# Kernel tuning notes

Measured on AMD Instinct MI355X. Metric: run time of the kernel, lower is better.

The kernel has to match this reference:

```python
import jax, jax.numpy as jnp
import numpy as np

B, E, D_IN, D = 4096, 8, 768, 768  # batch, num_domains, bert hidden, d_model


def setup_inputs() -> dict:
    key = jax.random.key(0)
    ks = jax.random.split(key, 10)
    rn = lambda k, sh: jax.random.normal(k, sh, dtype=jnp.float32) * 0.02
    zeros = lambda sh: jnp.zeros(sh, dtype=jnp.float32)
    return {
        "pooled": jax.random.normal(ks[0], (B, D_IN), dtype=jnp.float32),
        "domain_ids": jax.random.randint(ks[1], (B,), 0, E),
        # text_feature_extractor: Linear(768, d_model) + ReLU
        "W_tfe": rn(ks[2], (D_IN, D)), "b_tfe": zeros((D,)),
        # DomainFeatureExtractor per domain: FFN_1, FFN_2 (d->d each)
        "W1": rn(ks[3], (E, D, D)), "b1": zeros((E, D)),
        "W2": rn(ks[4], (E, D, D)), "b2": zeros((E, D)),
        # AdaptiveGate per domain: linear_1, linear_2 (d->d), gate_linear (2d->1)
        "G1": rn(ks[5], (E, D, D)), "g1b": zeros((E, D)),
        "G2": rn(ks[6], (E, D, D)), "g2b": zeros((E, D)),
        "Gg": rn(ks[7], (E, 2 * D)), "ggb": zeros((E,)),
    }


def reference(pooled, domain_ids, W_tfe, b_tfe, W1, b1, W2, b2,
              G1, g1b, G2, g2b, Gg, ggb):
    # text feature extractor (dropout = identity in eval)
    x = jax.nn.relu(pooled @ W_tfe + b_tfe)                        # [B, D]

    # Dense dispatch: compute every expert for every sample, then select.
    # Same math as the per-sample python loop in the torch module.
    h = jax.nn.relu(jnp.einsum('bd,edh->beh', x, W1) + b1)         # [B, E, D]
    df = jnp.einsum('beh,ehk->bek', h, W2) + b2                    # [B, E, D]

    # AdaptiveGate
    t = jax.nn.relu(jnp.einsum('bd,edh->beh', x, G1) + g1b)        # [B, E, D]
    dr = jax.nn.relu(jnp.einsum('bed,edh->beh', df, G2) + g2b)     # [B, E, D]
    # gate_linear on concat([t, dr]) == t @ Gg[:, :D] + dr @ Gg[:, D:]
    gl = (jnp.einsum('bed,ed->be', t, Gg[:, :D])
          + jnp.einsum('bed,ed->be', dr, Gg[:, D:]) + ggb)         # [B, E]
    gate = jax.nn.sigmoid(gl)                                      # [B, E]

    # route: pick this sample's domain expert
    b_idx = jnp.arange(x.shape[0])
    df_s = df[b_idx, domain_ids]                                   # [B, D]
    g_s = gate[b_idx, domain_ids][:, None]                         # [B, 1]

    final_feature = g_s * df_s + (1.0 - g_s) * x                   # [B, D]
    return final_feature
```

## Files before the change

kernel.cpp:

```cpp
#include <hip/hip_runtime.h>
#include <stdint.h>

#define BATCH 4096
#define NEXP 8
#define DIM 768
#define BM 128
#define BN 128
#define BK 32
#define MAXROWS (BATCH + NEXP * BM)
#define ROWBLKS (MAXROWS / BM)
#define COLBLKS (DIM / BN)
#define MATELEMS (DIM * DIM)

typedef __attribute__((ext_vector_type(4))) float f32x4;
typedef __attribute__((ext_vector_type(8))) __bf16 bf16x8;
typedef __attribute__((ext_vector_type(8))) unsigned short ushort8v;
typedef __attribute__((ext_vector_type(4))) unsigned short ushort4v;

__device__ __forceinline__ unsigned short f2bf(float f) {
  union { float f; unsigned u; } v; v.f = f;
  unsigned r = v.u + 0x7FFFu + ((v.u >> 16) & 1u);
  return (unsigned short)(r >> 16);
}
__device__ __forceinline__ float bf2f(unsigned short h) {
  union { unsigned u; float f; } v; v.u = ((unsigned)h) << 16;
  return v.f;
}

__global__ __launch_bounds__(256) void k_cvt(const float* __restrict__ src,
                                             unsigned short* __restrict__ dst, int n4) {
  int i = blockIdx.x * 256 + threadIdx.x;
  if (i >= n4) return;
  float4 v = *(const float4*)(src + (size_t)i * 4);
  ushort4v o = { f2bf(v.x), f2bf(v.y), f2bf(v.z), f2bf(v.w) };
  *(ushort4v*)(dst + (size_t)i * 4) = o;
}

__global__ __launch_bounds__(256) void k_transpose(
    const float* __restrict__ Wtfe, const float* __restrict__ W1,
    const float* __restrict__ W2, const float* __restrict__ G1,
    const float* __restrict__ G2, unsigned short* __restrict__ dst)
{
  __shared__ unsigned short lds[64][72];
  const int m = blockIdx.y;
  const float* src;
  if (m == 0)      src = Wtfe;
  else if (m < 9)  src = W1 + (size_t)(m - 1) * MATELEMS;
  else if (m < 17) src = W2 + (size_t)(m - 9) * MATELEMS;
  else if (m < 25) src = G1 + (size_t)(m - 17) * MATELEMS;
  else             src = G2 + (size_t)(m - 25) * MATELEMS;
  unsigned short* d = dst + (size_t)m * MATELEMS;
  const int r0 = (blockIdx.x / 12) * 64;
  const int c0 = (blockIdx.x % 12) * 64;
  const int t = threadIdx.x;
#pragma unroll
  for (int p = 0; p < 4; ++p) {
    int ri = p * 16 + (t >> 4);
    int ci = (t & 15) * 4;
    float4 v = *(const float4*)(src + (size_t)(r0 + ri) * DIM + c0 + ci);
    lds[ri][ci + 0] = f2bf(v.x);
    lds[ri][ci + 1] = f2bf(v.y);
    lds[ri][ci + 2] = f2bf(v.z);
    lds[ri][ci + 3] = f2bf(v.w);
  }
  __syncthreads();
#pragma unroll
  for (int p = 0; p < 2; ++p) {
    int jj = p * 32 + (t >> 3);
    int ii0 = (t & 7) * 8;
    ushort8v o;
#pragma unroll
    for (int u = 0; u < 8; ++u) o[u] = lds[ii0 + u][jj];
    *(ushort8v*)(d + (size_t)(c0 + jj) * DIM + r0 + ii0) = o;
  }
}

__global__ __launch_bounds__(256) void k_sort(const int* __restrict__ dom,
                                              int* __restrict__ seg,
                                              int* __restrict__ perm,
                                              float* __restrict__ gl) {
  __shared__ int cnt[8], cur[8], pstart[9];
  const int t = threadIdx.x;
  if (t < 8) { cnt[t] = 0; cur[t] = 0; }
  __syncthreads();
  for (int b = t; b < BATCH; b += 256) atomicAdd(&cnt[dom[b]], 1);
  __syncthreads();
  if (t == 0) {
    int acc = 0;
    for (int e = 0; e < 8; ++e) {
      pstart[e] = acc;
      acc += (cnt[e] + BM - 1) / BM * BM;
    }
    pstart[8] = acc;
    for (int e = 0; e < 9; ++e) seg[e] = pstart[e];
    for (int e = 0; e < 8; ++e) seg[9 + e] = cnt[e];
  }
  __syncthreads();
  for (int i = t; i < MAXROWS; i += 256) { perm[i] = 0; gl[i] = 0.0f; }
  __syncthreads();
  for (int b = t; b < BATCH; b += 256) {
    int e = dom[b];
    int pos = pstart[e] + atomicAdd(&cur[e], 1);
    perm[pos] = b;
  }
}

template <int MODE>
__global__ __launch_bounds__(256) void k_gemm(
    const unsigned short* __restrict__ A,
    const unsigned short* __restrict__ Wt,
    const float* __restrict__ bias,
    const float* __restrict__ Gg,
    const int* __restrict__ seg,
    const int* __restrict__ perm,
    unsigned short* __restrict__ Out,
    float* __restrict__ gl)
{
  __shared__ __align__(16) unsigned short lA[BM * BK];
  __shared__ __align__(16) unsigned short lB[BN * BK];

  const int i0 = blockIdx.x * BM;
  const int total = seg[8];
  if (i0 >= total) return;
  int e = 0;
#pragma unroll
  for (int q = 1; q < 8; ++q) if (i0 >= seg[q]) e = q;

  const int n0 = blockIdx.y * BN;
  const int t = threadIdx.x;
  const int lane = t & 63;
  const int w = t >> 6;
  const int wr = w >> 1, wc = w & 1;

  const unsigned short* We = Wt + (size_t)(MODE == 0 ? 0 : e) * MATELEMS;

  int grow[2];
#pragma unroll
  for (int c = 0; c < 2; ++c) {
    int sub = w * 2 + c;
    int row = sub * 16 + (lane >> 2);
    grow[c] = (MODE == 0) ? perm[i0 + row] : (i0 + row);
  }
  const int colb = (lane & 3) * 8;

  f32x4 acc[4][4];
#pragma unroll
  for (int mi = 0; mi < 4; ++mi)
#pragma unroll
    for (int ni = 0; ni < 4; ++ni) acc[mi][ni] = f32x4{0.f, 0.f, 0.f, 0.f};

  for (int kk = 0; kk < DIM; kk += BK) {
    ushort8v ta[2], tb[2];
#pragma unroll
    for (int c = 0; c < 2; ++c) {
      int sub = w * 2 + c;
      int brow = n0 + sub * 16 + (lane >> 2);
      ta[c] = *(const ushort8v*)(A + (size_t)grow[c] * DIM + kk + colb);
      tb[c] = *(const ushort8v*)(We + (size_t)brow * DIM + kk + colb);
    }
    __syncthreads();
#pragma unroll
    for (int c = 0; c < 2; ++c) {
      int sub = w * 2 + c;
      *(ushort8v*)(lA + sub * 512 + lane * 8) = ta[c];
      *(ushort8v*)(lB + sub * 512 + lane * 8) = tb[c];
    }
    __syncthreads();

    const int fr = lane & 15;
    const int kg = (lane >> 4) * 8;
    bf16x8 af[4], bfr[4];
#pragma unroll
    for (int mi = 0; mi < 4; ++mi) {
      ushort8v raw = *(const ushort8v*)(lA + (wr * 64 + mi * 16 + fr) * BK + kg);
      af[mi] = __builtin_bit_cast(bf16x8, raw);
    }
#pragma unroll
    for (int ni = 0; ni < 4; ++ni) {
      ushort8v raw = *(const ushort8v*)(lB + (wc * 64 + ni * 16 + fr) * BK + kg);
      bfr[ni] = __builtin_bit_cast(bf16x8, raw);
    }
#pragma unroll
    for (int mi = 0; mi < 4; ++mi)
#pragma unroll
      for (int ni = 0; ni < 4; ++ni)
        acc[mi][ni] = __builtin_amdgcn_mfma_f32_16x16x32_bf16(af[mi], bfr[ni], acc[mi][ni], 0, 0, 0);
  }

  const int fr = lane & 15;
  const int rg = (lane >> 4) * 4;

  if constexpr (MODE <= 2) {
#pragma unroll
    for (int mi = 0; mi < 4; ++mi) {
#pragma unroll
      for (int ni = 0; ni < 4; ++ni) {
        int gcol = n0 + wc * 64 + ni * 16 + fr;
        float bv = (MODE == 0) ? bias[gcol] : bias[e * DIM + gcol];
#pragma unroll
        for (int r = 0; r < 4; ++r) {
          int go = i0 + wr * 64 + mi * 16 + rg + r;
          float v = acc[mi][ni][r] + bv;
          if (MODE != 2) v = fmaxf(v, 0.0f);
          Out[(size_t)go * DIM + gcol] = f2bf(v);
        }
      }
    }
  } else {
    float psum[4][4];
#pragma unroll
    for (int mi = 0; mi < 4; ++mi)
#pragma unroll
      for (int r = 0; r < 4; ++r) psum[mi][r] = 0.0f;
#pragma unroll
    for (int mi = 0; mi < 4; ++mi) {
#pragma unroll
      for (int ni = 0; ni < 4; ++ni) {
        int gcol = n0 + wc * 64 + ni * 16 + fr;
        float bv = bias[e * DIM + gcol];
        float gg = Gg[e * 2 * DIM + (MODE == 4 ? DIM : 0) + gcol];
#pragma unroll
        for (int r = 0; r < 4; ++r) {
          float v = fmaxf(acc[mi][ni][r] + bv, 0.0f);
          psum[mi][r] += v * gg;
        }
      }
    }
#pragma unroll
    for (int s = 1; s < 16; s <<= 1)
#pragma unroll
      for (int mi = 0; mi < 4; ++mi)
#pragma unroll
        for (int r = 0; r < 4; ++r)
          psum[mi][r] += __shfl_xor(psum[mi][r], s, 64);
    if ((lane & 15) == 0) {
#pragma unroll
      for (int mi = 0; mi < 4; ++mi)
#pragma unroll
        for (int r = 0; r < 4; ++r)
          atomicAdd(&gl[i0 + wr * 64 + mi * 16 + rg + r], psum[mi][r]);
    }
  }
}

__global__ __launch_bounds__(256) void k_blend(
    const int* __restrict__ seg, const int* __restrict__ perm,
    const float* __restrict__ gl, const float* __restrict__ ggb,
    const unsigned short* __restrict__ xbf, const unsigned short* __restrict__ dfbf,
    float* __restrict__ out)
{
  int idx = blockIdx.x * 256 + threadIdx.x;
  int i = idx / 192;
  int q = idx % 192;
  if (i >= seg[8]) return;
  int e = 0;
#pragma unroll
  for (int p = 1; p < 8; ++p) if (i >= seg[p]) e = p;
  if (i - seg[e] >= seg[9 + e]) return;
  int b = perm[i];
  float z = gl[i] + ggb[e];
  float g = 1.0f / (1.0f + __expf(-z));
  ushort4v dv = *(const ushort4v*)(dfbf + (size_t)i * DIM + q * 4);
  ushort4v xv = *(const ushort4v*)(xbf + (size_t)i * DIM + q * 4);
  float4 o;
  o.x = g * bf2f(dv[0]) + (1.0f - g) * bf2f(xv[0]);
  o.y = g * bf2f(dv[1]) + (1.0f - g) * bf2f(xv[1]);
  o.z = g * bf2f(dv[2]) + (1.0f - g) * bf2f(xv[2]);
  o.w = g * bf2f(dv[3]) + (1.0f - g) * bf2f(xv[3]);
  *(float4*)(out + (size_t)b * DIM + q * 4) = o;
}

extern "C" void kernel_launch(void* const* d_in, const int* in_sizes, int n_in,
                              void* d_out, int out_size, void* d_ws, size_t ws_size,
                              hipStream_t stream)
{
  const float* pooled = (const float*)d_in[0];
  const int*   dom    = (const int*)d_in[1];
  const float* Wtfe   = (const float*)d_in[2];
  const float* btfe   = (const float*)d_in[3];
  const float* W1     = (const float*)d_in[4];
  const float* b1     = (const float*)d_in[5];
  const float* W2     = (const float*)d_in[6];
  const float* b2     = (const float*)d_in[7];
  const float* G1     = (const float*)d_in[8];
  const float* g1b    = (const float*)d_in[9];
  const float* G2     = (const float*)d_in[10];
  const float* g2b    = (const float*)d_in[11];
  const float* Gg     = (const float*)d_in[12];
  const float* ggb    = (const float*)d_in[13];
  float* out = (float*)d_out;

  char* w = (char*)d_ws;
  size_t o = 0;
  auto alloc = [&](size_t bytes) { char* p = w + o; o += (bytes + 255) & ~(size_t)255; return p; };
  int*            seg  = (int*)alloc(64 * 4);
  int*            perm = (int*)alloc(MAXROWS * 4);
  float*          gl   = (float*)alloc(MAXROWS * 4);
  unsigned short* pbf  = (unsigned short*)alloc((size_t)BATCH * DIM * 2);
  unsigned short* wt   = (unsigned short*)alloc((size_t)33 * MATELEMS * 2);
  unsigned short* xbf  = (unsigned short*)alloc((size_t)MAXROWS * DIM * 2);
  unsigned short* hbf  = (unsigned short*)alloc((size_t)MAXROWS * DIM * 2);
  unsigned short* dfbf = (unsigned short*)alloc((size_t)MAXROWS * DIM * 2);
  if (o > ws_size) return;

  k_cvt<<<(BATCH * DIM / 4 + 255) / 256, 256, 0, stream>>>(pooled, pbf, BATCH * DIM / 4);
  k_transpose<<<dim3(144, 33), 256, 0, stream>>>(Wtfe, W1, W2, G1, G2, wt);
  k_sort<<<1, 256, 0, stream>>>(dom, seg, perm, gl);

  dim3 gg(ROWBLKS, COLBLKS);
  k_gemm<0><<<gg, 256, 0, stream>>>(pbf,  wt,                          btfe, nullptr, seg, perm, xbf,  nullptr);
  k_gemm<1><<<gg, 256, 0, stream>>>(xbf,  wt + (size_t)1  * MATELEMS,  b1,   nullptr, seg, perm, hbf,  nullptr);
  k_gemm<2><<<gg, 256, 0, stream>>>(hbf,  wt + (size_t)9  * MATELEMS,  b2,   nullptr, seg, perm, dfbf, nullptr);
  k_gemm<3><<<gg, 256, 0, stream>>>(xbf,  wt + (size_t)17 * MATELEMS,  g1b,  Gg,      seg, perm, nullptr, gl);
  k_gemm<4><<<gg, 256, 0, stream>>>(dfbf, wt + (size_t)25 * MATELEMS,  g2b,  Gg,      seg, perm, nullptr, gl);

  k_blend<<<(MAXROWS * 192 + 255) / 256, 256, 0, stream>>>(seg, perm, gl, ggb, xbf, dfbf, out);
}
```

Before: 268.4 us.

## Fuse pooled conversion into first GEMM, merge FFN1 with gate GEMM, halve BM

The separate fp32-to-bf16 conversion kernel is removed, and the first GEMM now loads fp32 pooled rows directly and converts them in registers. The FFN_1 and gate linear_1 GEMMs, which both read x, are merged into one launch with a doubled column grid that picks the weight set per block. The row tile shrinks from 128 to 64, which cuts per-expert padding and doubles the block count. The cost is smaller per-block MFMA tiles with less A/B reuse, plus a strided fp32 gather in the first GEMM.

```diff
diff --git a/kernel.cpp b/kernel.cpp
--- a/kernel.cpp
+++ b/kernel.cpp
@@ -4,12 +4,11 @@
 #define BATCH 4096
 #define NEXP 8
 #define DIM 768
-#define BM 128
+#define BM 64
 #define BN 128
 #define BK 32
 #define MAXROWS (BATCH + NEXP * BM)
 #define ROWBLKS (MAXROWS / BM)
-#define COLBLKS (DIM / BN)
 #define MATELEMS (DIM * DIM)
 
 typedef __attribute__((ext_vector_type(4))) float f32x4;
@@ -25,15 +24,6 @@
 __device__ __forceinline__ float bf2f(unsigned short h) {
   union { unsigned u; float f; } v; v.u = ((unsigned)h) << 16;
   return v.f;
-}
-
-__global__ __launch_bounds__(256) void k_cvt(const float* __restrict__ src,
-                                             unsigned short* __restrict__ dst, int n4) {
-  int i = blockIdx.x * 256 + threadIdx.x;
-  if (i >= n4) return;
-  float4 v = *(const float4*)(src + (size_t)i * 4);
-  ushort4v o = { f2bf(v.x), f2bf(v.y), f2bf(v.z), f2bf(v.w) };
-  *(ushort4v*)(dst + (size_t)i * 4) = o;
 }
 
 __global__ __launch_bounds__(256) void k_transpose(
@@ -107,9 +97,11 @@
 
 template <int MODE>
 __global__ __launch_bounds__(256) void k_gemm(
-    const unsigned short* __restrict__ A,
-    const unsigned short* __restrict__ Wt,
-    const float* __restrict__ bias,
+    const void* __restrict__ Ain,
+    const unsigned short* __restrict__ Wa,
+    const float* __restrict__ ba,
+    const unsigned short* __restrict__ Wb,
+    const float* __restrict__ bb,
     const float* __restrict__ Gg,
     const int* __restrict__ seg,
     const int* __restrict__ perm,
@@ -120,86 +112,99 @@
   __shared__ __align__(16) unsigned short lB[BN * BK];
 
   const int i0 = blockIdx.x * BM;
-  const int total = seg[8];
-  if (i0 >= total) return;
+  if (i0 >= seg[8]) return;
   int e = 0;
 #pragma unroll
   for (int q = 1; q < 8; ++q) if (i0 >= seg[q]) e = q;
 
-  const int n0 = blockIdx.y * BN;
+  const bool isgate = (MODE == 3) || (MODE == 1 && blockIdx.y >= 6);
+  const int n0 = (MODE == 1 ? (int)(blockIdx.y % 6) : (int)blockIdx.y) * BN;
+
+  const unsigned short* We;
+  const float* bias;
+  if (MODE == 0) { We = Wa; bias = ba; }
+  else if (MODE == 1) {
+    We = (isgate ? Wb : Wa) + (size_t)e * MATELEMS;
+    bias = (isgate ? bb : ba) + e * DIM;
+  } else {
+    We = Wa + (size_t)e * MATELEMS;
+    bias = ba + e * DIM;
+  }
+
   const int t = threadIdx.x;
   const int lane = t & 63;
   const int w = t >> 6;
   const int wr = w >> 1, wc = w & 1;
-
-  const unsigned short* We = Wt + (size_t)(MODE == 0 ? 0 : e) * MATELEMS;
-
-  int grow[2];
-#pragma unroll
-  for (int c = 0; c < 2; ++c) {
-    int sub = w * 2 + c;
-    int row = sub * 16 + (lane >> 2);
-    grow[c] = (MODE == 0) ? perm[i0 + row] : (i0 + row);
-  }
+  const int srow = lane >> 2;
   const int colb = (lane & 3) * 8;
 
-  f32x4 acc[4][4];
-#pragma unroll
-  for (int mi = 0; mi < 4; ++mi)
+  const int arow_l = w * 16 + srow;
+  const int garow = (MODE == 0) ? perm[i0 + arow_l] : (i0 + arow_l);
+
+  const unsigned short* Abf = (const unsigned short*)Ain;
+  const float* Af32 = (const float*)Ain;
+
+  const int fr = lane & 15;
+  const int sl = lane >> 4;
+  const int kg = sl * 8;
+
+  f32x4 acc[2][4];
+#pragma unroll
+  for (int mi = 0; mi < 2; ++mi)
 #pragma unroll
     for (int ni = 0; ni < 4; ++ni) acc[mi][ni] = f32x4{0.f, 0.f, 0.f, 0.f};
 
   for (int kk = 0; kk < DIM; kk += BK) {
-    ushort8v ta[2], tb[2];
+    ushort8v ta, tb[2];
+    if (MODE == 0) {
+      float4 va0 = *(const float4*)(Af32 + (size_t)garow * DIM + kk + colb);
+      float4 va1 = *(const float4*)(Af32 + (size_t)garow * DIM + kk + colb + 4);
+      ta = ushort8v{ f2bf(va0.x), f2bf(va0.y), f2bf(va0.z), f2bf(va0.w),
+                     f2bf(va1.x), f2bf(va1.y), f2bf(va1.z), f2bf(va1.w) };
+    } else {
+      ta = *(const ushort8v*)(Abf + (size_t)garow * DIM + kk + colb);
+    }
 #pragma unroll
     for (int c = 0; c < 2; ++c) {
-      int sub = w * 2 + c;
-      int brow = n0 + sub * 16 + (lane >> 2);
-      ta[c] = *(const ushort8v*)(A + (size_t)grow[c] * DIM + kk + colb);
+      int brow = n0 + (w * 2 + c) * 16 + srow;
       tb[c] = *(const ushort8v*)(We + (size_t)brow * DIM + kk + colb);
     }
     __syncthreads();
-#pragma unroll
-    for (int c = 0; c < 2; ++c) {
-      int sub = w * 2 + c;
-      *(ushort8v*)(lA + sub * 512 + lane * 8) = ta[c];
-      *(ushort8v*)(lB + sub * 512 + lane * 8) = tb[c];
-    }
+    *(ushort8v*)(lA + arow_l * 32 + colb) = ta;
+#pragma unroll
+    for (int c = 0; c < 2; ++c)
+      *(ushort8v*)(lB + ((w * 2 + c) * 16 + srow) * 32 + colb) = tb[c];
     __syncthreads();
 
-    const int fr = lane & 15;
-    const int kg = (lane >> 4) * 8;
-    bf16x8 af[4], bfr[4];
-#pragma unroll
-    for (int mi = 0; mi < 4; ++mi) {
-      ushort8v raw = *(const ushort8v*)(lA + (wr * 64 + mi * 16 + fr) * BK + kg);
+    bf16x8 af[2], bfv[4];
+#pragma unroll
+    for (int mi = 0; mi < 2; ++mi) {
+      ushort8v raw = *(const ushort8v*)(lA + (wr * 32 + mi * 16 + fr) * 32 + kg);
       af[mi] = __builtin_bit_cast(bf16x8, raw);
     }
 #pragma unroll
     for (int ni = 0; ni < 4; ++ni) {
-      ushort8v raw = *(const ushort8v*)(lB + (wc * 64 + ni * 16 + fr) * BK + kg);
-      bfr[ni] = __builtin_bit_cast(bf16x8, raw);
-    }
-#pragma unroll
-    for (int mi = 0; mi < 4; ++mi)
+      ushort8v raw = *(const ushort8v*)(lB + (wc * 64 + ni * 16 + fr) * 32 + kg);
+      bfv[ni] = __builtin_bit_cast(bf16x8, raw);
+    }
+#pragma unroll
+    for (int mi = 0; mi < 2; ++mi)
 #pragma unroll
       for (int ni = 0; ni < 4; ++ni)
-        acc[mi][ni] = __builtin_amdgcn_mfma_f32_16x16x32_bf16(af[mi], bfr[ni], acc[mi][ni], 0, 0, 0);
-  }
-
-  const int fr = lane & 15;
-  const int rg = (lane >> 4) * 4;
-
-  if constexpr (MODE <= 2) {
-#pragma unroll
-    for (int mi = 0; mi < 4; ++mi) {
+        acc[mi][ni] = __builtin_amdgcn_mfma_f32_16x16x32_bf16(af[mi], bfv[ni], acc[mi][ni], 0, 0, 0);
+  }
+
+  const int rg = sl * 4;
+  if (!isgate) {
+#pragma unroll
+    for (int mi = 0; mi < 2; ++mi) {
 #pragma unroll
       for (int ni = 0; ni < 4; ++ni) {
         int gcol = n0 + wc * 64 + ni * 16 + fr;
-        float bv = (MODE == 0) ? bias[gcol] : bias[e * DIM + gcol];
+        float bv = bias[gcol];
 #pragma unroll
         for (int r = 0; r < 4; ++r) {
-          int go = i0 + wr * 64 + mi * 16 + rg + r;
+          int go = i0 + wr * 32 + mi * 16 + rg + r;
           float v = acc[mi][ni][r] + bv;
           if (MODE != 2) v = fmaxf(v, 0.0f);
           Out[(size_t)go * DIM + gcol] = f2bf(v);
@@ -207,38 +212,37 @@
       }
     }
   } else {
-    float psum[4][4];
-#pragma unroll
-    for (int mi = 0; mi < 4; ++mi)
+    const int goff = (MODE == 3) ? DIM : 0;
+    float psum[2][4];
+#pragma unroll
+    for (int mi = 0; mi < 2; ++mi)
 #pragma unroll
       for (int r = 0; r < 4; ++r) psum[mi][r] = 0.0f;
 #pragma unroll
-    for (int mi = 0; mi < 4; ++mi) {
+    for (int mi = 0; mi < 2; ++mi) {
 #pragma unroll
       for (int ni = 0; ni < 4; ++ni) {
         int gcol = n0 + wc * 64 + ni * 16 + fr;
-        float bv = bias[e * DIM + gcol];
-        float gg = Gg[e * 2 * DIM + (MODE == 4 ? DIM : 0) + gcol];
-#pragma unroll
-        for (int r = 0; r < 4; ++r) {
-          float v = fmaxf(acc[mi][ni][r] + bv, 0.0f);
-          psum[mi][r] += v * gg;
-        }
+        float bv = bias[gcol];
+        float gg = Gg[e * 2 * DIM + goff + gcol];
+#pragma unroll
+        for (int r = 0; r < 4; ++r)
+          psum[mi][r] += fmaxf(acc[mi][ni][r] + bv, 0.0f) * gg;
       }
     }
 #pragma unroll
     for (int s = 1; s < 16; s <<= 1)
 #pragma unroll
-      for (int mi = 0; mi < 4; ++mi)
+      for (int mi = 0; mi < 2; ++mi)
 #pragma unroll
         for (int r = 0; r < 4; ++r)
           psum[mi][r] += __shfl_xor(psum[mi][r], s, 64);
-    if ((lane & 15) == 0) {
-#pragma unroll
-      for (int mi = 0; mi < 4; ++mi)
+    if (fr == 0) {
+#pragma unroll
+      for (int mi = 0; mi < 2; ++mi)
 #pragma unroll
         for (int r = 0; r < 4; ++r)
-          atomicAdd(&gl[i0 + wr * 64 + mi * 16 + rg + r], psum[mi][r]);
+          atomicAdd(&gl[i0 + wr * 32 + mi * 16 + rg + r], psum[mi][r]);
     }
   }
 }
@@ -296,23 +300,25 @@
   int*            seg  = (int*)alloc(64 * 4);
   int*            perm = (int*)alloc(MAXROWS * 4);
   float*          gl   = (float*)alloc(MAXROWS * 4);
-  unsigned short* pbf  = (unsigned short*)alloc((size_t)BATCH * DIM * 2);
   unsigned short* wt   = (unsigned short*)alloc((size_t)33 * MATELEMS * 2);
   unsigned short* xbf  = (unsigned short*)alloc((size_t)MAXROWS * DIM * 2);
   unsigned short* hbf  = (unsigned short*)alloc((size_t)MAXROWS * DIM * 2);
   unsigned short* dfbf = (unsigned short*)alloc((size_t)MAXROWS * DIM * 2);
   if (o > ws_size) return;
 
-  k_cvt<<<(BATCH * DIM / 4 + 255) / 256, 256, 0, stream>>>(pooled, pbf, BATCH * DIM / 4);
   k_transpose<<<dim3(144, 33), 256, 0, stream>>>(Wtfe, W1, W2, G1, G2, wt);
   k_sort<<<1, 256, 0, stream>>>(dom, seg, perm, gl);
 
-  dim3 gg(ROWBLKS, COLBLKS);
-  k_gemm<0><<<gg, 256, 0, stream>>>(pbf,  wt,                          btfe, nullptr, seg, perm, xbf,  nullptr);
-  k_gemm<1><<<gg, 256, 0, stream>>>(xbf,  wt + (size_t)1  * MATELEMS,  b1,   nullptr, seg, perm, hbf,  nullptr);
-  k_gemm<2><<<gg, 256, 0, stream>>>(hbf,  wt + (size_t)9  * MATELEMS,  b2,   nullptr, seg, perm, dfbf, nullptr);
-  k_gemm<3><<<gg, 256, 0, stream>>>(xbf,  wt + (size_t)17 * MATELEMS,  g1b,  Gg,      seg, perm, nullptr, gl);
-  k_gemm<4><<<gg, 256, 0, stream>>>(dfbf, wt + (size_t)25 * MATELEMS,  g2b,  Gg,      seg, perm, nullptr, gl);
+  const unsigned short* wt0  = wt;
+  const unsigned short* wt1  = wt + (size_t)1  * MATELEMS;
+  const unsigned short* wt2  = wt + (size_t)9  * MATELEMS;
+  const unsigned short* wtg1 = wt + (size_t)17 * MATELEMS;
+  const unsigned short* wtg2 = wt + (size_t)25 * MATELEMS;
+
+  k_gemm<0><<<dim3(ROWBLKS, 6),  256, 0, stream>>>(pooled, wt0,  btfe, nullptr, nullptr, Gg, seg, perm, xbf,  gl);
+  k_gemm<1><<<dim3(ROWBLKS, 12), 256, 0, stream>>>(xbf,    wt1,  b1,   wtg1,    g1b,     Gg, seg, perm, hbf,  gl);
+  k_gemm<2><<<dim3(ROWBLKS, 6),  256, 0, stream>>>(hbf,    wt2,  b2,   nullptr, nullptr, Gg, seg, perm, dfbf, gl);
+  k_gemm<3><<<dim3(ROWBLKS, 6),  256, 0, stream>>>(dfbf,   wtg2, g2b,  nullptr, nullptr, Gg, seg, perm, nullptr, gl);
 
   k_blend<<<(MAXROWS * 192 + 255) / 256, 256, 0, stream>>>(seg, perm, gl, ggb, xbf, dfbf, out);
 }
```

Result: faster. 260.7 us (-2.9%).
